# Kernel tuning notes

Measured on AMD Instinct MI355X. Metric: run time of the kernel, lower is better.

Reference implementation:

```python
import jax, jax.numpy as jnp
import numpy as np

N, F_IN, H, D = 4096, 256, 4, 64  # out_features = H*D = 256
SLOPE = 0.2
LN_EPS = 1e-5


def setup_inputs() -> dict:
    key = jax.random.key(0)
    k1, k2, k3, k4 = jax.random.split(key, 4)
    x = jax.random.normal(k1, (N, F_IN), dtype=jnp.float32)
    adjacency = jax.random.bernoulli(k2, 0.5, (N, N))
    # xavier_uniform for W [H*D, F_IN] and a [H, 2*D]
    lim_w = float(np.sqrt(6.0 / (F_IN + H * D)))
    W = jax.random.uniform(k3, (H * D, F_IN), minval=-lim_w, maxval=lim_w, dtype=jnp.float32)
    lim_a = float(np.sqrt(6.0 / (H + 2 * D)))
    a = jax.random.uniform(k4, (H, 2 * D), minval=-lim_a, maxval=lim_a, dtype=jnp.float32)
    ln_gamma = jnp.ones((H * D,), dtype=jnp.float32)
    ln_beta = jnp.zeros((H * D,), dtype=jnp.float32)
    return {"x": x, "adjacency": adjacency, "W": W, "a": a,
            "ln_gamma": ln_gamma, "ln_beta": ln_beta}


def _layernorm(y, gamma, beta):
    mu = jnp.mean(y, axis=-1, keepdims=True)
    var = jnp.mean((y - mu) ** 2, axis=-1, keepdims=True)
    return (y - mu) * jax.lax.rsqrt(var + LN_EPS) * gamma + beta


def reference(x, adjacency, W, a, ln_gamma, ln_beta):
    # Wx: [N, H, D]
    Wx = (x @ W.T).reshape(N, H, D)
    # Additive score split: sum over concat([Wx_i, Wx_j]) * a == Wx_i.a_src + Wx_j.a_dst
    a_src, a_dst = a[:, :D], a[:, D:]
    s_i = jnp.einsum('nhd,hd->nh', Wx, a_src)  # [N, H] (destination i)
    s_j = jnp.einsum('nhd,hd->nh', Wx, a_dst)  # [N, H] (source j)
    e = s_i[:, None, :] + s_j[None, :, :]       # [N, N, H]
    e = jnp.where(e >= 0, e, SLOPE * e)          # leaky relu
    e = jnp.where(adjacency[:, :, None], e, -jnp.inf)
    attn = jax.nn.softmax(e, axis=1)             # softmax over source j (dim=1)
    # dropout is identity in eval mode
    out = jnp.einsum('ijh,jhd->ihd', attn, Wx).reshape(N, H * D)
    out = out + x  # out_features == in_features -> residual
    return _layernorm(out, ln_gamma, ln_beta)
```

## Files before the change

### kernel.cpp

```cpp
#include <hip/hip_runtime.h>
#include <hip/hip_bf16.h>
#include <cstdint>
#include <cstddef>

#define N_NODES 4096
#define F_IN    256
#define H_HEADS 4
#define D_HEAD  64
#define FEAT    256
#define SLOPE   0.2f
#define LN_EPS  1e-5f

#define NCHUNK  4
#define J_CHUNK 1024
#define I_TILE  32
#define K_STEP  32
#define NSTEP   (J_CHUNK / K_STEP)

typedef __attribute__((ext_vector_type(8))) short bf16x8;
typedef __attribute__((ext_vector_type(4))) float f32x4;

#define GMAX_OFF   64
#define ADJB_OFF   256
#define ADJB_BYTES ((size_t)N_NODES * 128 * 4)
#define WXT_OFF    (ADJB_OFF + ADJB_BYTES)
#define WXT_BYTES  ((size_t)FEAT * N_NODES * 2)
#define SSRC_OFF   (WXT_OFF + WXT_BYTES)
#define SVEC_BYTES ((size_t)H_HEADS * N_NODES * 4)
#define ETAB_OFF   (SSRC_OFF + SVEC_BYTES)
#define ETAB_BYTES ((size_t)H_HEADS * N_NODES * 8)
#define WSL_OFF    (ETAB_OFF + ETAB_BYTES)
#define WSL_BYTES  ((size_t)NCHUNK * N_NODES * H_HEADS * 4)
#define WSACC_OFF  (WSL_OFF + WSL_BYTES)

__device__ __forceinline__ short f2bf(float f) {
    uint32_t u = __float_as_uint(f);
    uint32_t r = (u + 0x7fffu + ((u >> 16) & 1u)) >> 16;
    return (short)r;
}
__device__ __forceinline__ uint32_t fkey(float f) {
    uint32_t u = __float_as_uint(f);
    return ((int)u < 0) ? ~u : (u | 0x80000000u);
}
__device__ __forceinline__ float funkey(uint32_t k) {
    uint32_t u = (k & 0x80000000u) ? (k & 0x7fffffffu) : ~k;
    return __uint_as_float(u);
}

__global__ __launch_bounds__(256) void pack_adj(const void* __restrict__ adjv,
                                                uint32_t* __restrict__ bits,
                                                uint32_t* __restrict__ gmax) {
    __shared__ int s_u8;
    const int t   = threadIdx.x;
    const int gid = blockIdx.x * 256 + t;
    if (blockIdx.x == 0 && t < H_HEADS) gmax[t] = 0u;

    uint32_t w8[8];
    const uint32_t* src8 = (const uint32_t*)adjv + (size_t)gid * 8;
    #pragma unroll
    for (int k = 0; k < 8; ++k) w8[k] = src8[k];

    uint32_t off = 0;
    #pragma unroll
    for (int k = 0; k < 8; ++k) off |= (w8[k] & 0xFFFFFF00u);
    if (t == 0) s_u8 = 0;
    __syncthreads();
    if (off) s_u8 = 1;
    __syncthreads();

    uint32_t b = 0;
    if (s_u8) {
        #pragma unroll
        for (int k = 0; k < 8; ++k) {
            uint32_t v = w8[k];
            if (v & 0x000000ffu) b |= 1u << (k * 4 + 0);
            if (v & 0x0000ff00u) b |= 1u << (k * 4 + 1);
            if (v & 0x00ff0000u) b |= 1u << (k * 4 + 2);
            if (v & 0xff000000u) b |= 1u << (k * 4 + 3);
        }
    } else {
        const int4* src = (const int4*)adjv + (size_t)gid * 8;
        #pragma unroll
        for (int k = 0; k < 8; ++k) {
            int4 v = src[k];
            if (v.x) b |= 1u << (k * 4 + 0);
            if (v.y) b |= 1u << (k * 4 + 1);
            if (v.z) b |= 1u << (k * 4 + 2);
            if (v.w) b |= 1u << (k * 4 + 3);
        }
    }
    bits[gid] = b;
}

__global__ __launch_bounds__(256) void gemm_wx(const float* __restrict__ x,
                                               const float* __restrict__ W,
                                               const float* __restrict__ a,
                                               short* __restrict__ WxT,
                                               float* __restrict__ s_srcT,
                                               float2* __restrict__ etab,
                                               uint32_t* __restrict__ gmax) {
    __shared__ float xs[64][68];
    __shared__ float wsm[64][68];
    __shared__ float aS[64], aD[64];
    __shared__ float wredmax[4];
    const int h  = blockIdx.x;
    const int nt = blockIdx.y;
    const int t  = threadIdx.x;
    const int tm = t >> 4, tn = t & 15;
    if (t < 64)       aS[t]      = a[h * 128 + t];
    else if (t < 128) aD[t - 64] = a[h * 128 + 64 + (t - 64)];
    float acc[4][4] = {};

    for (int k0 = 0; k0 < F_IN; k0 += 64) {
        #pragma unroll
        for (int s = 0; s < 4; ++s) {
            int idx = t + s * 256;
            int r = idx >> 4, c4 = (idx & 15) << 2;
            *(float4*)&xs[r][c4]  = *(const float4*)&x[(size_t)(nt * 64 + r) * F_IN + k0 + c4];
            *(float4*)&wsm[r][c4] = *(const float4*)&W[(size_t)(h * 64 + r) * F_IN + k0 + c4];
        }
        __syncthreads();
        #pragma unroll 4
        for (int kq = 0; kq < 16; ++kq) {
            float4 xa[4], wb[4];
            #pragma unroll
            for (int mi = 0; mi < 4; ++mi) xa[mi] = *(const float4*)&xs[tm * 4 + mi][kq * 4];
            #pragma unroll
            for (int ni = 0; ni < 4; ++ni) wb[ni] = *(const float4*)&wsm[tn + 16 * ni][kq * 4];
            #pragma unroll
            for (int mi = 0; mi < 4; ++mi)
                #pragma unroll
                for (int ni = 0; ni < 4; ++ni) {
                    acc[mi][ni] = fmaf(xa[mi].x, wb[ni].x, acc[mi][ni]);
                    acc[mi][ni] = fmaf(xa[mi].y, wb[ni].y, acc[mi][ni]);
                    acc[mi][ni] = fmaf(xa[mi].z, wb[ni].z, acc[mi][ni]);
                    acc[mi][ni] = fmaf(xa[mi].w, wb[ni].w, acc[mi][ni]);
                }
        }
        __syncthreads();
    }

    #pragma unroll
    for (int ni = 0; ni < 4; ++ni) {
        short4 sv;
        sv.x = f2bf(acc[0][ni]); sv.y = f2bf(acc[1][ni]);
        sv.z = f2bf(acc[2][ni]); sv.w = f2bf(acc[3][ni]);
        *(short4*)&WxT[(size_t)(h * 64 + tn + 16 * ni) * N_NODES + nt * 64 + tm * 4] = sv;
    }

    float ps[4] = {0.f, 0.f, 0.f, 0.f}, pd[4] = {0.f, 0.f, 0.f, 0.f};
    #pragma unroll
    for (int mi = 0; mi < 4; ++mi)
        #pragma unroll
        for (int ni = 0; ni < 4; ++ni) {
            float v = acc[mi][ni];
            ps[mi] = fmaf(v, aS[tn + 16 * ni], ps[mi]);
            pd[mi] = fmaf(v, aD[tn + 16 * ni], pd[mi]);
        }
    #pragma unroll
    for (int o = 1; o < 16; o <<= 1) {
        #pragma unroll
        for (int mi = 0; mi < 4; ++mi) {
            ps[mi] += __shfl_xor(ps[mi], o, 64);
            pd[mi] += __shfl_xor(pd[mi], o, 64);
        }
    }
    float lmax = -INFINITY;
    if (tn == 0) {
        #pragma unroll
        for (int mi = 0; mi < 4; ++mi) {
            int node = nt * 64 + tm * 4 + mi;
            s_srcT[(size_t)h * N_NODES + node] = ps[mi];
            etab[(size_t)h * N_NODES + node] = make_float2(__expf(pd[mi]), __expf(0.2f * pd[mi]));
            lmax = fmaxf(lmax, pd[mi]);
        }
    }
    #pragma unroll
    for (int o = 1; o < 64; o <<= 1) lmax = fmaxf(lmax, __shfl_xor(lmax, o, 64));
    if ((t & 63) == 0) wredmax[t >> 6] = lmax;
    __syncthreads();
    if (t == 0) {
        float m = fmaxf(fmaxf(wredmax[0], wredmax[1]), fmaxf(wredmax[2], wredmax[3]));
        atomicMax(&gmax[h], fkey(m));
    }
}

__global__ __launch_bounds__(512, 4) void attn_chunk(const short* __restrict__ WxT,
                                                     const float* __restrict__ s_srcT,
                                                     const float2* __restrict__ etab,
                                                     const uint32_t* __restrict__ adjbits,
                                                     const uint32_t* __restrict__ gmax,
                                                     float* __restrict__ ws_l,
                                                     float* __restrict__ ws_acc) {
    __shared__ short    Bt[2][256][40];
    __shared__ uint32_t adjW[32][33];
    __shared__ float    EJ[4 * 2048];

    const int t     = threadIdx.x;
    const int tile  = blockIdx.x >> 2;
    const int chunk = blockIdx.x & 3;
    const int i0    = tile * I_TILE;
    const int jc    = chunk * J_CHUNK;
    const int wave  = t >> 6, lane = t & 63;
    const int h     = wave & 3, mh = wave >> 2;
    const int col   = lane & 15, q = lane >> 4;

    for (int s2 = t; s2 < 1024; s2 += 512)
        adjW[s2 >> 5][s2 & 31] =
            adjbits[(size_t)(i0 + (s2 >> 5)) * 128 + chunk * 32 + (s2 & 31)];
    {
        const float4* esrc = (const float4*)etab;
        for (int s2 = t; s2 < 2048; s2 += 512) {
            int pl = s2 >> 9, off = s2 & 511;
            *(float4*)&EJ[pl * 2048 + off * 4] = esrc[(size_t)pl * 2048 + (jc >> 1) + off];
        }
    }

    const int sf = t >> 1, shalf = t & 1;
    const int4* gsrc = (const int4*)(WxT + (size_t)sf * N_NODES + jc);
    int4 pfA0, pfA1, pfB0, pfB1;
    pfA0 = gsrc[shalf * 2 + 0];           pfA1 = gsrc[shalf * 2 + 1];
    pfB0 = gsrc[4 + shalf * 2 + 0];       pfB1 = gsrc[4 + shalf * 2 + 1];
    {
        int4* ld = (int4*)&Bt[0][sf][shalf * 16];
        ld[0] = pfA0; ld[1] = pfA1;
    }
    __syncthreads();

    const int   iL  = mh * 16 + col;
    const int   i   = i0 + iL;
    const float si  = s_srcT[(size_t)h * N_NODES + i];
    const float gm  = funkey(gmax[h]);
    const float em0 = si + gm;
    const float mi_ = fmaxf(em0, SLOPE * em0);
    const float Ai  = __expf(si - mi_);
    const float A2i = __expf(0.2f * si - mi_);
    const float Ti  = __expf(-si);

    f32x4 cacc[4], cl;
    #pragma unroll
    for (int n = 0; n < 4; ++n)
        #pragma unroll
        for (int r2 = 0; r2 < 4; ++r2) cacc[n][r2] = 0.f;
    #pragma unroll
    for (int r2 = 0; r2 < 4; ++r2) cl[r2] = 0.f;

    bf16x8 onesf;
    #pragma unroll
    for (int e = 0; e < 8; ++e) onesf[e] = (col == 0) ? (short)0x3F80 : (short)0;

    #pragma unroll 2
    for (int ks = 0; ks < NSTEP; ++ks) {
        const int cur = ks & 1;

        if (ks + 1 < NSTEP) {
            int4* ld = (int4*)&Bt[cur ^ 1][sf][shalf * 16];
            if (cur) { ld[0] = pfA0; ld[1] = pfA1; }
            else     { ld[0] = pfB0; ld[1] = pfB1; }
        }
        if (ks + 2 < NSTEP) {
            if (cur) { pfB0 = gsrc[(ks + 2) * 4 + shalf * 2]; pfB1 = gsrc[(ks + 2) * 4 + shalf * 2 + 1]; }
            else     { pfA0 = gsrc[(ks + 2) * 4 + shalf * 2]; pfA1 = gsrc[(ks + 2) * 4 + shalf * 2 + 1]; }
        }

        uint32_t wq = adjW[iL][ks] >> (q * 8);
        float ej[16];
        {
            const float* eb = &EJ[h * 2048 + (ks * 32 + q * 8) * 2];
            *(float4*)&ej[0]  = *(const float4*)&eb[0];
            *(float4*)&ej[4]  = *(const float4*)&eb[4];
            *(float4*)&ej[8]  = *(const float4*)&eb[8];
            *(float4*)&ej[12] = *(const float4*)&eb[12];
        }
        union { uint32_t w[4]; bf16x8 v; } apu;
        #pragma unroll
        for (int pp = 0; pp < 4; ++pp) {
            float B0 = ej[4 * pp + 0], B20 = ej[4 * pp + 1];
            bool pos0 = B0 >= Ti;
            float pv0 = (pos0 ? Ai : A2i) * (pos0 ? B0 : B20);
            pv0 = (wq & (1u << (2 * pp))) ? pv0 : 0.f;
            float B1 = ej[4 * pp + 2], B21 = ej[4 * pp + 3];
            bool pos1 = B1 >= Ti;
            float pv1 = (pos1 ? Ai : A2i) * (pos1 ? B1 : B21);
            pv1 = (wq & (1u << (2 * pp + 1))) ? pv1 : 0.f;
            apu.w[pp] = __builtin_amdgcn_perm(__float_as_uint(pv1), __float_as_uint(pv0),
                                              0x07060302u);
        }

        #pragma unroll
        for (int n = 0; n < 4; ++n) {
            bf16x8 bfr = *(const bf16x8*)&Bt[cur][h * 64 + n * 16 + col][q * 8];
            cacc[n] = __builtin_amdgcn_mfma_f32_16x16x32_bf16(apu.v, bfr, cacc[n], 0, 0, 0);
        }
        cl = __builtin_amdgcn_mfma_f32_16x16x32_bf16(apu.v, onesf, cl, 0, 0, 0);

        __syncthreads();
    }

    #pragma unroll
    for (int n = 0; n < 4; ++n)
        #pragma unroll
        for (int r = 0; r < 4; ++r) {
            int ii = i0 + mh * 16 + q * 4 + r;
            ws_acc[((size_t)chunk * N_NODES + ii) * FEAT + h * 64 + n * 16 + col] = cacc[n][r];
        }
    if (col == 0) {
        #pragma unroll
        for (int r = 0; r < 4; ++r) {
            int ii = i0 + mh * 16 + q * 4 + r;
            ws_l[((size_t)chunk * N_NODES + ii) * H_HEADS + h] = cl[r];
        }
    }
}

__global__ __launch_bounds__(256) void finalize_kernel(const float* __restrict__ x,
                                                       const float* __restrict__ gamma,
                                                       const float* __restrict__ beta,
                                                       const float* __restrict__ ws_l,
                                                       const float* __restrict__ ws_acc,
                                                       float* __restrict__ out) {
    const int w    = threadIdx.x >> 6;
    const int lane = threadIdx.x & 63;
    const int i    = blockIdx.x * 4 + w;
    const int h    = lane >> 4;

    float L = 0.f;
    float4 y = make_float4(0.f, 0.f, 0.f, 0.f);
    #pragma unroll
    for (int c = 0; c < NCHUNK; ++c) {
        L += ws_l[((size_t)c * N_NODES + i) * H_HEADS + h];
        float4 v = *(const float4*)&ws_acc[((size_t)c * N_NODES + i) * FEAT + lane * 4];
        y.x += v.x; y.y += v.y; y.z += v.z; y.w += v.w;
    }
    float inv = (L > 0.f) ? (1.f / L) : 0.f;
    float4 xv = *(const float4*)&x[(size_t)i * FEAT + lane * 4];
    y.x = y.x * inv + xv.x; y.y = y.y * inv + xv.y;
    y.z = y.z * inv + xv.z; y.w = y.w * inv + xv.w;

    float s1 = y.x + y.y + y.z + y.w;
    float s2 = y.x * y.x + y.y * y.y + y.z * y.z + y.w * y.w;
    #pragma unroll
    for (int o = 32; o > 0; o >>= 1) {
        s1 += __shfl_xor(s1, o, 64);
        s2 += __shfl_xor(s2, o, 64);
    }
    float mu  = s1 * (1.f / 256.f);
    float var = s2 * (1.f / 256.f) - mu * mu;
    float r = 1.0f / sqrtf(var + LN_EPS);
    float4 g = *(const float4*)&gamma[lane * 4];
    float4 b = *(const float4*)&beta[lane * 4];
    float4 o4;
    o4.x = (y.x - mu) * r * g.x + b.x;
    o4.y = (y.y - mu) * r * g.y + b.y;
    o4.z = (y.z - mu) * r * g.z + b.z;
    o4.w = (y.w - mu) * r * g.w + b.w;
    *(float4*)&out[(size_t)i * FEAT + lane * 4] = o4;
}

extern "C" void kernel_launch(void* const* d_in, const int* in_sizes, int n_in,
                              void* d_out, int out_size, void* d_ws, size_t ws_size,
                              hipStream_t stream) {
    const float* x     = (const float*)d_in[0];
    const void*  adj   = d_in[1];
    const float* W     = (const float*)d_in[2];
    const float* a     = (const float*)d_in[3];
    const float* gamma = (const float*)d_in[4];
    const float* beta  = (const float*)d_in[5];
    float* out = (float*)d_out;

    char* ws = (char*)d_ws;
    uint32_t* gmax    = (uint32_t*)(ws + GMAX_OFF);
    uint32_t* adjbits = (uint32_t*)(ws + ADJB_OFF);
    short*    WxT     = (short*)(ws + WXT_OFF);
    float*    s_srcT  = (float*)(ws + SSRC_OFF);
    float2*   etab    = (float2*)(ws + ETAB_OFF);
    float*    ws_l    = (float*)(ws + WSL_OFF);
    float*    ws_acc  = (float*)(ws + WSACC_OFF);

    pack_adj<<<2048, 256, 0, stream>>>(adj, adjbits, gmax);
    gemm_wx<<<dim3(4, 64), 256, 0, stream>>>(x, W, a, WxT, s_srcT, etab, gmax);
    attn_chunk<<<512, 512, 0, stream>>>(WxT, s_srcT, etab, adjbits, gmax, ws_l, ws_acc);
    finalize_kernel<<<1024, 256, 0, stream>>>(x, gamma, beta, ws_l, ws_acc, out);
}
```

Measured before the change: 159.8 us.

## Merge prep kernels, split source dimension into eight chunks, read exp table from global

Merges adjacency packing and the Wx GEMM into one launch, with each packing thread handling four words. The global max becomes per-block partial maxima that attn_chunk reduces with shuffles, replacing the atomic and its zero-init ordering. The attention grid doubles to 1024 blocks with 512-column chunks and a higher occupancy hint. The exp table is now read directly from global memory instead of being staged in LDS. This cuts a launch and LDS use to raise occupancy and parallelism, at the cost of more partial results for finalize to combine and uncached global loads in the inner loop.

```diff
diff --git a/kernel.cpp b/kernel.cpp
--- a/kernel.cpp
+++ b/kernel.cpp
@@ -11,8 +11,8 @@
 #define SLOPE   0.2f
 #define LN_EPS  1e-5f
 
-#define NCHUNK  4
-#define J_CHUNK 1024
+#define NCHUNK  8
+#define J_CHUNK 512
 #define I_TILE  32
 #define K_STEP  32
 #define NSTEP   (J_CHUNK / K_STEP)
@@ -21,7 +21,7 @@
 typedef __attribute__((ext_vector_type(4))) float f32x4;
 
 #define GMAX_OFF   64
-#define ADJB_OFF   256
+#define ADJB_OFF   4096
 #define ADJB_BYTES ((size_t)N_NODES * 128 * 4)
 #define WXT_OFF    (ADJB_OFF + ADJB_BYTES)
 #define WXT_BYTES  ((size_t)FEAT * N_NODES * 2)
@@ -38,74 +38,72 @@
     uint32_t r = (u + 0x7fffu + ((u >> 16) & 1u)) >> 16;
     return (short)r;
 }
-__device__ __forceinline__ uint32_t fkey(float f) {
-    uint32_t u = __float_as_uint(f);
-    return ((int)u < 0) ? ~u : (u | 0x80000000u);
-}
-__device__ __forceinline__ float funkey(uint32_t k) {
-    uint32_t u = (k & 0x80000000u) ? (k & 0x7fffffffu) : ~k;
-    return __uint_as_float(u);
-}
-
-__global__ __launch_bounds__(256) void pack_adj(const void* __restrict__ adjv,
-                                                uint32_t* __restrict__ bits,
-                                                uint32_t* __restrict__ gmax) {
-    __shared__ int s_u8;
-    const int t   = threadIdx.x;
-    const int gid = blockIdx.x * 256 + t;
-    if (blockIdx.x == 0 && t < H_HEADS) gmax[t] = 0u;
-
-    uint32_t w8[8];
-    const uint32_t* src8 = (const uint32_t*)adjv + (size_t)gid * 8;
-    #pragma unroll
-    for (int k = 0; k < 8; ++k) w8[k] = src8[k];
-
-    uint32_t off = 0;
-    #pragma unroll
-    for (int k = 0; k < 8; ++k) off |= (w8[k] & 0xFFFFFF00u);
-    if (t == 0) s_u8 = 0;
-    __syncthreads();
-    if (off) s_u8 = 1;
-    __syncthreads();
-
-    uint32_t b = 0;
-    if (s_u8) {
-        #pragma unroll
-        for (int k = 0; k < 8; ++k) {
-            uint32_t v = w8[k];
-            if (v & 0x000000ffu) b |= 1u << (k * 4 + 0);
-            if (v & 0x0000ff00u) b |= 1u << (k * 4 + 1);
-            if (v & 0x00ff0000u) b |= 1u << (k * 4 + 2);
-            if (v & 0xff000000u) b |= 1u << (k * 4 + 3);
-        }
-    } else {
-        const int4* src = (const int4*)adjv + (size_t)gid * 8;
-        #pragma unroll
-        for (int k = 0; k < 8; ++k) {
-            int4 v = src[k];
-            if (v.x) b |= 1u << (k * 4 + 0);
-            if (v.y) b |= 1u << (k * 4 + 1);
-            if (v.z) b |= 1u << (k * 4 + 2);
-            if (v.w) b |= 1u << (k * 4 + 3);
-        }
-    }
-    bits[gid] = b;
-}
-
-__global__ __launch_bounds__(256) void gemm_wx(const float* __restrict__ x,
-                                               const float* __restrict__ W,
-                                               const float* __restrict__ a,
-                                               short* __restrict__ WxT,
-                                               float* __restrict__ s_srcT,
-                                               float2* __restrict__ etab,
-                                               uint32_t* __restrict__ gmax) {
+
+__global__ __launch_bounds__(256) void prep_kernel(const void* __restrict__ adjv,
+                                                   uint32_t* __restrict__ bits,
+                                                   const float* __restrict__ x,
+                                                   const float* __restrict__ W,
+                                                   const float* __restrict__ a,
+                                                   short* __restrict__ WxT,
+                                                   float* __restrict__ s_srcT,
+                                                   float2* __restrict__ etab,
+                                                   float* __restrict__ gmaxArr) {
+    __shared__ int   s_u8;
     __shared__ float xs[64][68];
     __shared__ float wsm[64][68];
     __shared__ float aS[64], aD[64];
     __shared__ float wredmax[4];
-    const int h  = blockIdx.x;
-    const int nt = blockIdx.y;
-    const int t  = threadIdx.x;
+
+    const int bid = blockIdx.x;
+    const int t   = threadIdx.x;
+
+    if (bid < 512) {
+        const int gid4 = (bid * 256 + t) * 4;
+        uint32_t w8[32];
+        const uint32_t* s8 = (const uint32_t*)adjv + (size_t)gid4 * 8;
+        uint32_t off = 0;
+        #pragma unroll
+        for (int k = 0; k < 32; ++k) { w8[k] = s8[k]; off |= w8[k] & 0xFFFFFF00u; }
+        if (t == 0) s_u8 = 0;
+        __syncthreads();
+        if (off) s_u8 = 1;
+        __syncthreads();
+
+        if (s_u8) {
+            #pragma unroll
+            for (int w = 0; w < 4; ++w) {
+                uint32_t b = 0;
+                #pragma unroll
+                for (int k = 0; k < 8; ++k) {
+                    uint32_t v = w8[w * 8 + k];
+                    if (v & 0x000000ffu) b |= 1u << (k * 4 + 0);
+                    if (v & 0x0000ff00u) b |= 1u << (k * 4 + 1);
+                    if (v & 0x00ff0000u) b |= 1u << (k * 4 + 2);
+                    if (v & 0xff000000u) b |= 1u << (k * 4 + 3);
+                }
+                bits[gid4 + w] = b;
+            }
+        } else {
+            const int4* si = (const int4*)adjv + (size_t)gid4 * 8;
+            #pragma unroll
+            for (int w = 0; w < 4; ++w) {
+                uint32_t b = 0;
+                #pragma unroll
+                for (int k = 0; k < 8; ++k) {
+                    int4 v = si[w * 8 + k];
+                    if (v.x) b |= 1u << (k * 4 + 0);
+                    if (v.y) b |= 1u << (k * 4 + 1);
+                    if (v.z) b |= 1u << (k * 4 + 2);
+                    if (v.w) b |= 1u << (k * 4 + 3);
+                }
+                bits[gid4 + w] = b;
+            }
+        }
+        return;
+    }
+
+    const int h  = (bid - 512) >> 6;
+    const int nt = (bid - 512) & 63;
     const int tm = t >> 4, tn = t & 15;
     if (t < 64)       aS[t]      = a[h * 128 + t];
     else if (t < 128) aD[t - 64] = a[h * 128 + 64 + (t - 64)];
@@ -181,40 +179,30 @@
     __syncthreads();
     if (t == 0) {
         float m = fmaxf(fmaxf(wredmax[0], wredmax[1]), fmaxf(wredmax[2], wredmax[3]));
-        atomicMax(&gmax[h], fkey(m));
-    }
-}
-
-__global__ __launch_bounds__(512, 4) void attn_chunk(const short* __restrict__ WxT,
+        gmaxArr[h * 64 + nt] = m;
+    }
+}
+
+__global__ __launch_bounds__(512, 6) void attn_chunk(const short* __restrict__ WxT,
                                                      const float* __restrict__ s_srcT,
                                                      const float2* __restrict__ etab,
                                                      const uint32_t* __restrict__ adjbits,
-                                                     const uint32_t* __restrict__ gmax,
+                                                     const float* __restrict__ gmaxArr,
                                                      float* __restrict__ ws_l,
                                                      float* __restrict__ ws_acc) {
     __shared__ short    Bt[2][256][40];
-    __shared__ uint32_t adjW[32][33];
-    __shared__ float    EJ[4 * 2048];
+    __shared__ uint32_t adjW[32][17];
 
     const int t     = threadIdx.x;
-    const int tile  = blockIdx.x >> 2;
-    const int chunk = blockIdx.x & 3;
+    const int tile  = blockIdx.x >> 3;
+    const int chunk = blockIdx.x & 7;
     const int i0    = tile * I_TILE;
     const int jc    = chunk * J_CHUNK;
     const int wave  = t >> 6, lane = t & 63;
     const int h     = wave & 3, mh = wave >> 2;
     const int col   = lane & 15, q = lane >> 4;
 
-    for (int s2 = t; s2 < 1024; s2 += 512)
-        adjW[s2 >> 5][s2 & 31] =
-            adjbits[(size_t)(i0 + (s2 >> 5)) * 128 + chunk * 32 + (s2 & 31)];
-    {
-        const float4* esrc = (const float4*)etab;
-        for (int s2 = t; s2 < 2048; s2 += 512) {
-            int pl = s2 >> 9, off = s2 & 511;
-            *(float4*)&EJ[pl * 2048 + off * 4] = esrc[(size_t)pl * 2048 + (jc >> 1) + off];
-        }
-    }
+    adjW[t >> 4][t & 15] = adjbits[(size_t)(i0 + (t >> 4)) * 128 + chunk * 16 + (t & 15)];
 
     const int sf = t >> 1, shalf = t & 1;
     const int4* gsrc = (const int4*)(WxT + (size_t)sf * N_NODES + jc);
@@ -227,15 +215,20 @@
     }
     __syncthreads();
 
+    float gv = gmaxArr[h * 64 + lane];
+    #pragma unroll
+    for (int o = 1; o < 64; o <<= 1) gv = fmaxf(gv, __shfl_xor(gv, o, 64));
+    const float gm  = gv;
+
     const int   iL  = mh * 16 + col;
     const int   i   = i0 + iL;
     const float si  = s_srcT[(size_t)h * N_NODES + i];
-    const float gm  = funkey(gmax[h]);
     const float em0 = si + gm;
     const float mi_ = fmaxf(em0, SLOPE * em0);
     const float Ai  = __expf(si - mi_);
     const float A2i = __expf(0.2f * si - mi_);
     const float Ti  = __expf(-si);
+    const float4* ejg = (const float4*)(etab + (size_t)h * N_NODES);
 
     f32x4 cacc[4], cl;
     #pragma unroll
@@ -264,22 +257,18 @@
         }
 
         uint32_t wq = adjW[iL][ks] >> (q * 8);
-        float ej[16];
-        {
-            const float* eb = &EJ[h * 2048 + (ks * 32 + q * 8) * 2];
-            *(float4*)&ej[0]  = *(const float4*)&eb[0];
-            *(float4*)&ej[4]  = *(const float4*)&eb[4];
-            *(float4*)&ej[8]  = *(const float4*)&eb[8];
-            *(float4*)&ej[12] = *(const float4*)&eb[12];
-        }
+        const int fb = (jc + ks * 32 + q * 8) >> 1;
+        float4 e4[4];
+        e4[0] = ejg[fb]; e4[1] = ejg[fb + 1]; e4[2] = ejg[fb + 2]; e4[3] = ejg[fb + 3];
+
         union { uint32_t w[4]; bf16x8 v; } apu;
         #pragma unroll
         for (int pp = 0; pp < 4; ++pp) {
-            float B0 = ej[4 * pp + 0], B20 = ej[4 * pp + 1];
+            float B0 = e4[pp].x, B20 = e4[pp].y;
             bool pos0 = B0 >= Ti;
             float pv0 = (pos0 ? Ai : A2i) * (pos0 ? B0 : B20);
             pv0 = (wq & (1u << (2 * pp))) ? pv0 : 0.f;
-            float B1 = ej[4 * pp + 2], B21 = ej[4 * pp + 3];
+            float B1 = e4[pp].z, B21 = e4[pp].w;
             bool pos1 = B1 >= Ti;
             float pv1 = (pos1 ? Ai : A2i) * (pos1 ? B1 : B21);
             pv1 = (wq & (1u << (2 * pp + 1))) ? pv1 : 0.f;
@@ -369,7 +358,7 @@
     float* out = (float*)d_out;
 
     char* ws = (char*)d_ws;
-    uint32_t* gmax    = (uint32_t*)(ws + GMAX_OFF);
+    float*    gmaxArr = (float*)(ws + GMAX_OFF);
     uint32_t* adjbits = (uint32_t*)(ws + ADJB_OFF);
     short*    WxT     = (short*)(ws + WXT_OFF);
     float*    s_srcT  = (float*)(ws + SSRC_OFF);
@@ -377,8 +366,7 @@
     float*    ws_l    = (float*)(ws + WSL_OFF);
     float*    ws_acc  = (float*)(ws + WSACC_OFF);
 
-    pack_adj<<<2048, 256, 0, stream>>>(adj, adjbits, gmax);
-    gemm_wx<<<dim3(4, 64), 256, 0, stream>>>(x, W, a, WxT, s_srcT, etab, gmax);
-    attn_chunk<<<512, 512, 0, stream>>>(WxT, s_srcT, etab, adjbits, gmax, ws_l, ws_acc);
+    prep_kernel<<<768, 256, 0, stream>>>(adj, adjbits, x, W, a, WxT, s_srcT, etab, gmaxArr);
+    attn_chunk<<<1024, 512, 0, stream>>>(WxT, s_srcT, etab, adjbits, gmaxArr, ws_l, ws_acc);
     finalize_kernel<<<1024, 256, 0, stream>>>(x, gamma, beta, ws_l, ws_acc, out);
 }
```

New measurement: 177.5 us. 1.11x slower.
